# Performance work log

Hardware: AMD Instinct MI355X
Metric: run time of the kernel (lower is better)

## Reference

```python
import jax, jax.numpy as jnp
import numpy as np

B, T, H, V = 32, 16, 768, 32000
EPS = 1e-5


def _conv(x, w, stride, pad):
    return jax.lax.conv_general_dilated(
        x, w, (stride, stride), [(pad, pad), (pad, pad)],
        dimension_numbers=('NCHW', 'OIHW', 'NCHW'))


def _bn(x, g, b, m, v):
    inv = g / jnp.sqrt(v + EPS)
    return x * inv[None, :, None, None] + (b - m * inv)[None, :, None, None]


def setup_inputs() -> dict:
    key = jax.random.key(0)
    ks = iter(jax.random.split(key, 48))

    def rn(shape, s=0.02):
        return s * jax.random.normal(next(ks), shape, jnp.float32)

    def bn_params(c):
        g = 1.0 + 0.1 * jax.random.normal(next(ks), (c,), jnp.float32)
        b = 0.1 * jax.random.normal(next(ks), (c,), jnp.float32)
        m = 0.1 * jax.random.normal(next(ks), (c,), jnp.float32)
        v = jax.random.uniform(next(ks), (c,), jnp.float32, 0.5, 1.5)
        return g, b, m, v

    inp = {}
    inp['images'] = jax.random.normal(next(ks), (B, 3, 224, 224), jnp.float32)
    inp['captions'] = jax.random.randint(next(ks), (B, T), 0, V)

    inp['conv1_w'] = rn((64, 3, 7, 7))
    inp['bn1_g'], inp['bn1_b'], inp['bn1_m'], inp['bn1_v'] = bn_params(64)
    inp['conv2_w'] = rn((128, 64, 3, 3))
    inp['bn2_g'], inp['bn2_b'], inp['bn2_m'], inp['bn2_v'] = bn_params(128)
    inp['conv3_w'] = rn((256, 128, 3, 3))
    inp['bn3_g'], inp['bn3_b'], inp['bn3_m'], inp['bn3_v'] = bn_params(256)
    inp['conv4_w'] = rn((H, 256, 3, 3))
    inp['bn4_g'], inp['bn4_b'], inp['bn4_m'], inp['bn4_v'] = bn_params(H)

    emb = rn((V, H), 1.0)
    inp['emb_table'] = emb.at[0].set(0.0)  # padding_idx=0 row is zero
    inp['attn_w'] = rn((H, H))             # attn_proj (no bias)
    inp['w_ih'] = rn((4 * H, 2 * H))       # LSTM input weights (i,f,g,o)
    inp['w_hh'] = rn((4 * H, H))
    inp['b_ih'] = rn((4 * H,))
    inp['b_hh'] = rn((4 * H,))
    inp['fc_w'] = rn((V, H))
    inp['fc_b'] = rn((V,))
    return inp


def _forward(images, captions, conv1_w, bn1_g, bn1_b, bn1_m, bn1_v,
             conv2_w, bn2_g, bn2_b, bn2_m, bn2_v,
             conv3_w, bn3_g, bn3_b, bn3_m, bn3_v,
             conv4_w, bn4_g, bn4_b, bn4_m, bn4_v,
             emb_table, attn_w, w_ih, w_hh, b_ih, b_hh, fc_w, fc_b):
    # ---- ResNetEncoder ----
    x = jax.nn.relu(_bn(_conv(images, conv1_w, 2, 3), bn1_g, bn1_b, bn1_m, bn1_v))
    x = jax.lax.reduce_window(x, -jnp.inf, jax.lax.max, (1, 1, 3, 3), (1, 1, 2, 2),
                              ((0, 0), (0, 0), (1, 1), (1, 1)))
    x = jax.nn.relu(_bn(_conv(x, conv2_w, 1, 1), bn2_g, bn2_b, bn2_m, bn2_v))
    x = jax.nn.relu(_bn(_conv(x, conv3_w, 2, 1), bn3_g, bn3_b, bn3_m, bn3_v))
    x = jax.nn.relu(_bn(_conv(x, conv4_w, 1, 1), bn4_g, bn4_b, bn4_m, bn4_v))
    b, c, hh, ww = x.shape
    memory = x.reshape(b, c, hh * ww).transpose(0, 2, 1)[:, :196, :]  # [B,196,H]

    # ---- LSTMAttnDecoder ----
    emb = emb_table[captions]  # [B,T,H]
    h0 = jnp.zeros((b, H), jnp.float32)
    c0 = jnp.zeros((b, H), jnp.float32)

    def step(carry, e_t):
        h, cst = carry
        q = h @ attn_w.T                                    # [B,H]
        scores = jnp.einsum('bh,bmh->bm', q, memory)        # [B,196]
        ctx = jnp.einsum('bm,bmh->bh', jax.nn.softmax(scores, axis=-1), memory)
        xin = jnp.concatenate([e_t, ctx], axis=-1)          # [B,2H]
        gates = xin @ w_ih.T + b_ih + h @ w_hh.T + b_hh     # [B,4H]
        i, f, g, o = jnp.split(gates, 4, axis=-1)
        c_new = jax.nn.sigmoid(f) * cst + jax.nn.sigmoid(i) * jnp.tanh(g)
        h_new = jax.nn.sigmoid(o) * jnp.tanh(c_new)
        logits = h_new @ fc_w.T + fc_b                      # [B,V]
        return (h_new, c_new), logits

    (hT, cT), logits = jax.lax.scan(step, (h0, c0), emb.transpose(1, 0, 2))
    logits = logits.transpose(1, 0, 2)  # [B,T,V]
    return logits, (hT[None], cT[None])


def reference(images, captions, conv1_w, bn1_g, bn1_b, bn1_m, bn1_v,
              conv2_w, bn2_g, bn2_b, bn2_m, bn2_v,
              conv3_w, bn3_g, bn3_b, bn3_m, bn3_v,
              conv4_w, bn4_g, bn4_b, bn4_m, bn4_v,
              emb_table, attn_w, w_ih, w_hh, b_ih, b_hh, fc_w, fc_b):
    return _forward(images, captions, conv1_w, bn1_g, bn1_b, bn1_m, bn1_v,
                    conv2_w, bn2_g, bn2_b, bn2_m, bn2_v,
                    conv3_w, bn3_g, bn3_b, bn3_m, bn3_v,
                    conv4_w, bn4_g, bn4_b, bn4_m, bn4_v,
                    emb_table, attn_w, w_ih, w_hh, b_ih, b_hh, fc_w, fc_b)
```

## Files before the change

### kernel.cpp

```cpp
#include <hip/hip_runtime.h>
#include <math.h>

#define NB 32
#define NT 16
#define NH 768
#define NV 32000

typedef short bf16x8 __attribute__((ext_vector_type(8)));
typedef float floatx4 __attribute__((ext_vector_type(4)));
typedef unsigned short ushort_t;

__device__ __forceinline__ float bf2f(unsigned short h) {
    unsigned u = ((unsigned)h) << 16;
    return __builtin_bit_cast(float, u);
}
__device__ __forceinline__ unsigned short f2bf(float f) {
    unsigned u = __builtin_bit_cast(unsigned, f);
    u += 0x7fffu + ((u >> 16) & 1u);
    return (unsigned short)(u >> 16);
}
__device__ __forceinline__ float sigmoidf_(float x) { return 1.f / (1.f + expf(-x)); }

__device__ __forceinline__ int swz8(int bid, int N) {
    return (bid & 7) * (N >> 3) + (bid >> 3);
}

__device__ __forceinline__ bf16x8 cvt8(float4 a, float4 b) {
    bf16x8 t;
    t[0] = (short)f2bf(a.x); t[1] = (short)f2bf(a.y);
    t[2] = (short)f2bf(a.z); t[3] = (short)f2bf(a.w);
    t[4] = (short)f2bf(b.x); t[5] = (short)f2bf(b.y);
    t[6] = (short)f2bf(b.z); t[7] = (short)f2bf(b.w);
    return t;
}

__global__ __launch_bounds__(256) void bn_prep4(
    const float* __restrict__ g1, const float* __restrict__ b1, const float* __restrict__ m1, const float* __restrict__ v1,
    const float* __restrict__ g2, const float* __restrict__ b2, const float* __restrict__ m2, const float* __restrict__ v2,
    const float* __restrict__ g3, const float* __restrict__ b3, const float* __restrict__ m3, const float* __restrict__ v3,
    const float* __restrict__ g4, const float* __restrict__ b4, const float* __restrict__ m4, const float* __restrict__ v4,
    float* __restrict__ s1, float* __restrict__ o1, float* __restrict__ s2, float* __restrict__ o2,
    float* __restrict__ s3, float* __restrict__ o3, float* __restrict__ s4, float* __restrict__ o4) {
    int i = blockIdx.x * 256 + threadIdx.x;
    const float *g, *b, *m, *v;
    float *s, *o;
    int c;
    if (i < 64)        { g = g1; b = b1; m = m1; v = v1; s = s1; o = o1; c = i; }
    else if (i < 192)  { g = g2; b = b2; m = m2; v = v2; s = s2; o = o2; c = i - 64; }
    else if (i < 448)  { g = g3; b = b3; m = m3; v = v3; s = s3; o = o3; c = i - 192; }
    else if (i < 1216) { g = g4; b = b4; m = m4; v = v4; s = s4; o = o4; c = i - 448; }
    else return;
    float inv = g[c] * rsqrtf(v[c] + 1e-5f);
    s[c] = inv;
    o[c] = b[c] - m[c] * inv;
}

__global__ __launch_bounds__(256) void zfill(unsigned long long* __restrict__ p, long long n) {
    long long i = (long long)blockIdx.x * 256 + threadIdx.x;
    if (i < n) p[i] = 0ULL;
}

__global__ __launch_bounds__(256) void cvt_b16rows(const float* __restrict__ src, ushort_t* __restrict__ dst,
                                                   int cols8, int ldsrc, int total8) {
    int i = blockIdx.x * 256 + threadIdx.x;
    if (i >= total8) return;
    int r = i / cols8, g = i % cols8;
    const float4* s = (const float4*)(src + (size_t)r * ldsrc + g * 8);
    float4 a = s[0], b = s[1];
    *(bf16x8*)(dst + (size_t)i * 8) = cvt8(a, b);
}

__global__ __launch_bounds__(256) void cvt_packW_conv(const float* __restrict__ w, ushort_t* __restrict__ dst,
                                                      int CIN, int total) {
    int idx = blockIdx.x * 256 + threadIdx.x;
    if (idx >= total) return;
    int e = idx & 7, lane = (idx >> 3) & 63, j = (idx >> 9) & 3;
    int r = idx >> 11;
    int KQ = CIN >> 5;
    int kq = r % KQ; r /= KQ;
    int tap = r % 9; int nt = r / 9;
    int co = nt * 64 + j * 16 + (lane & 15);
    int ci = kq * 32 + (lane >> 4) * 8 + e;
    dst[idx] = f2bf(w[((size_t)co * CIN + ci) * 9 + tap]);
}

__global__ __launch_bounds__(256) void cvt_wcombP(const float* __restrict__ w_ih, const float* __restrict__ w_hh,
                                                  ushort_t* __restrict__ dst) {
    int idx = blockIdx.x * 256 + threadIdx.x;
    if (idx >= 3072 * 1536) return;
    int e = idx & 7, lane = (idx >> 3) & 63;
    int t = idx >> 9;
    int kq = t % 48, gg = t / 48;
    int g = gg & 3, bx = gg >> 2;
    int j = g * 768 + bx * 16 + (lane & 15);
    int k = kq * 32 + (lane >> 4) * 8 + e;
    float v = (k < NH) ? w_ih[(size_t)j * (2 * NH) + NH + k] : w_hh[(size_t)j * NH + (k - NH)];
    dst[idx] = f2bf(v);
}

__global__ __launch_bounds__(256) void cvt_wattnTP(const float* __restrict__ w, ushort_t* __restrict__ dst) {
    int idx = blockIdx.x * 256 + threadIdx.x;
    if (idx >= 768 * 768) return;
    int e = idx & 7, lane = (idx >> 3) & 63, j = (idx >> 9) & 3;
    int t = idx >> 11;
    int kq = t % 24, nt = t / 24;
    int n = nt * 64 + 16 * j + (lane & 15);
    int k = kq * 32 + (lane >> 4) * 8 + e;
    dst[idx] = f2bf(w[(size_t)k * 768 + n]);
}

__global__ __launch_bounds__(256) void cvt_pad(const float* __restrict__ src, ushort_t* __restrict__ dst) {
    int idx = blockIdx.x * 256 + threadIdx.x;
    if (idx >= 64 * 160) return;
    int co = idx / 160, k = idx % 160;
    dst[idx] = (k < 147) ? f2bf(src[co * 147 + k]) : (ushort_t)0;
}

__global__ __launch_bounds__(256) void im2col1(const float* __restrict__ img, ushort_t* __restrict__ A) {
    int idx = blockIdx.x * 256 + threadIdx.x;
    const int total = 121856 * 160;
    if (idx >= total) return;
    int k = idx % 160;
    int m = idx / 160;
    ushort_t v = 0;
    if (k < 147) {
        int b = m / 3808;
        int rm = m % 3808;
        int y = rm / 112, x = rm % 112;
        int ci = k / 49;
        int r = k % 49;
        int ky = r / 7, kx = r % 7;
        int iy = 2 * y - 3 + ky;
        int ix = 2 * x - 3 + kx;
        if ((unsigned)iy < 224u && (unsigned)ix < 224u)
            v = f2bf(img[((size_t)(b * 3 + ci) * 224 + iy) * 224 + ix]);
    }
    A[idx] = v;
}

__global__ __launch_bounds__(256) void conv1_gemm(
    const ushort_t* __restrict__ A, const ushort_t* __restrict__ Bw,
    const float* __restrict__ scale, const float* __restrict__ bias,
    ushort_t* __restrict__ out) {
    int lane = threadIdx.x & 63, w = threadIdx.x >> 6;
    int m0 = (blockIdx.x * 4 + w) * 64;
    int lr = lane & 15, kl = (lane >> 4) * 8;
    floatx4 acc[4][4];
    #pragma unroll
    for (int i = 0; i < 4; ++i)
        #pragma unroll
        for (int j = 0; j < 4; ++j) acc[i][j] = 0.f;
    #pragma unroll
    for (int k0 = 0; k0 < 160; k0 += 32) {
        bf16x8 a[4], bb[4];
        #pragma unroll
        for (int i = 0; i < 4; ++i) a[i] = *(const bf16x8*)(A + (size_t)(m0 + 16 * i + lr) * 160 + kl + k0);
        #pragma unroll
        for (int j = 0; j < 4; ++j) bb[j] = *(const bf16x8*)(Bw + (size_t)(16 * j + lr) * 160 + kl + k0);
        #pragma unroll
        for (int i = 0; i < 4; ++i)
            #pragma unroll
            for (int j = 0; j < 4; ++j)
                acc[i][j] = __builtin_amdgcn_mfma_f32_16x16x32_bf16(a[i], bb[j], acc[i][j], 0, 0, 0);
    }
    #pragma unroll
    for (int i = 0; i < 4; ++i) {
        #pragma unroll
        for (int r = 0; r < 4; ++r) {
            int m = m0 + 16 * i + (lane >> 4) * 4 + r;
            int b = m / 3808;
            int rm = m % 3808;
            int y = rm / 112, x = rm % 112;
            #pragma unroll
            for (int j = 0; j < 4; ++j) {
                int n = 16 * j + lr;
                float v = fmaxf(acc[i][j][r] * scale[n] + bias[n], 0.f);
                out[((size_t)(b * 34 + y) * 112 + x) * 64 + n] = f2bf(v);
            }
        }
    }
}

__global__ __launch_bounds__(256) void pool_kernel(const ushort_t* __restrict__ in,
                                                   ushort_t* __restrict__ hal2) {
    int idx = blockIdx.x * 256 + threadIdx.x;
    const int total = 32 * 17 * 56 * 8;
    if (idx >= total) return;
    int c8 = idx & 7;
    int rest = idx >> 3;
    int x = rest % 56; rest /= 56;
    int y = rest % 17; int b = rest / 17;
    float mx[8];
    #pragma unroll
    for (int j = 0; j < 8; ++j) mx[j] = -INFINITY;
    for (int dy = -1; dy <= 1; ++dy) {
        int iy = 2 * y + dy;
        if ((unsigned)iy >= 34u) continue;
        for (int dx = -1; dx <= 1; ++dx) {
            int ix = 2 * x + dx;
            if ((unsigned)ix >= 112u) continue;
            bf16x8 v = *(const bf16x8*)(in + (((size_t)(b * 34 + iy)) * 112 + ix) * 64 + c8 * 8);
            #pragma unroll
            for (int j = 0; j < 8; ++j) mx[j] = fmaxf(mx[j], bf2f((unsigned short)v[j]));
        }
    }
    bf16x8 o;
    #pragma unroll
    for (int j = 0; j < 8; ++j) o[j] = (short)f2bf(mx[j]);
    *(bf16x8*)(hal2 + (((size_t)(b * 19 + y + 1)) * 58 + (x + 1)) * 64 + c8 * 8) = o;
}

template <int CIN, int HH, int WH, int STRIDE, int HOUT, int WOUT, int COUT, int MEMOUT, int OH, int OW>
__global__ __launch_bounds__(64) void conv_mfma(
    const ushort_t* __restrict__ in, const ushort_t* __restrict__ wtP,
    const float* __restrict__ scale, const float* __restrict__ bias,
    ushort_t* __restrict__ out) {
    const int KQ = CIN / 32;
    const int NK = 9 * KQ;
    const int MT = (32 * HOUT * WOUT) / 64;
    const int NTL = COUT / 64;
    int id = swz8(blockIdx.x, MT * NTL);
    int mt = id % MT, nt = id / MT;
    int lane = threadIdx.x;
    int lr = lane & 15, kl = (lane >> 4) * 8;
    int rowoff[4];
    #pragma unroll
    for (int i = 0; i < 4; ++i) {
        int m = mt * 64 + 16 * i + lr;
        int b = m / (HOUT * WOUT);
        int rm = m % (HOUT * WOUT);
        int y = rm / WOUT, x = rm % WOUT;
        rowoff[i] = ((b * HH + y * STRIDE) * WH + x * STRIDE) * CIN + kl;
    }
    floatx4 acc[4][4];
    #pragma unroll
    for (int i = 0; i < 4; ++i)
        #pragma unroll
        for (int j = 0; j < 4; ++j) acc[i][j] = 0.f;

    auto ioffOf = [&](int ks) {
        int tap = ks / KQ;
        int k0 = (ks & (KQ - 1)) * 32;
        int ky = tap / 3, kx = tap - ky * 3;
        return (ky * WH + kx) * CIN + k0;
    };
    const ushort_t* bbase = wtP + ((size_t)nt * 9 * KQ * 4 * 64 + lane) * 8;

    bf16x8 aC[4], bC[4], aN[4], bN[4];
    {
        int io = ioffOf(0);
        #pragma unroll
        for (int i = 0; i < 4; ++i) aC[i] = *(const bf16x8*)(in + rowoff[i] + io);
        #pragma unroll
        for (int j = 0; j < 4; ++j) bC[j] = *(const bf16x8*)(bbase + ((size_t)(0 * 4 + j) * 64) * 8);
    }
    for (int ks = 0; ks < NK; ks += 2) {
        {
            int io = ioffOf(ks + 1);
            #pragma unroll
            for (int i = 0; i < 4; ++i) aN[i] = *(const bf16x8*)(in + rowoff[i] + io);
            #pragma unroll
            for (int j = 0; j < 4; ++j) bN[j] = *(const bf16x8*)(bbase + ((size_t)((ks + 1) * 4 + j) * 64) * 8);
        }
        #pragma unroll
        for (int i = 0; i < 4; ++i)
            #pragma unroll
            for (int j = 0; j < 4; ++j)
                acc[i][j] = __builtin_amdgcn_mfma_f32_16x16x32_bf16(aC[i], bC[j], acc[i][j], 0, 0, 0);
        if (ks + 2 < NK) {
            int io = ioffOf(ks + 2);
            #pragma unroll
            for (int i = 0; i < 4; ++i) aC[i] = *(const bf16x8*)(in + rowoff[i] + io);
            #pragma unroll
            for (int j = 0; j < 4; ++j) bC[j] = *(const bf16x8*)(bbase + ((size_t)((ks + 2) * 4 + j) * 64) * 8);
        }
        #pragma unroll
        for (int i = 0; i < 4; ++i)
            #pragma unroll
            for (int j = 0; j < 4; ++j)
                acc[i][j] = __builtin_amdgcn_mfma_f32_16x16x32_bf16(aN[i], bN[j], acc[i][j], 0, 0, 0);
    }
    #pragma unroll
    for (int i = 0; i < 4; ++i) {
        #pragma unroll
        for (int r = 0; r < 4; ++r) {
            int m = mt * 64 + 16 * i + (lane >> 4) * 4 + r;
            int b = m / (HOUT * WOUT);
            int rm = m % (HOUT * WOUT);
            int y = rm / WOUT, x = rm % WOUT;
            #pragma unroll
            for (int j = 0; j < 4; ++j) {
                int n = nt * 64 + 16 * j + lr;
                float v = fmaxf(acc[i][j][r] * scale[n] + bias[n], 0.f);
                ushort_t hv = f2bf(v);
                if (MEMOUT) {
                    out[(size_t)m * COUT + n] = hv;
                } else {
                    out[((size_t)(b * OH + y + 1) * OW + (x + 1)) * COUT + n] = hv;
                }
            }
        }
    }
}

__global__ __launch_bounds__(64) void kmat_gemm(
    const ushort_t* __restrict__ memv, const ushort_t* __restrict__ Bp,
    ushort_t* __restrict__ KT) {
    int id = swz8(blockIdx.x, 98 * 12);
    int mt = id % 98, nt = id / 98;
    int lane = threadIdx.x;
    int lr = lane & 15, kl = (lane >> 4) * 8;
    const ushort_t* arow[4];
    #pragma unroll
    for (int i = 0; i < 4; ++i) arow[i] = memv + (size_t)(mt * 64 + 16 * i + lr) * 768 + kl;
    const ushort_t* bbase = Bp + ((size_t)nt * 24 * 4 * 64 + lane) * 8;
    floatx4 acc[4][4];
    #pragma unroll
    for (int i = 0; i < 4; ++i)
        #pragma unroll
        for (int j = 0; j < 4; ++j) acc[i][j] = 0.f;
    bf16x8 aC[4], bC[4], aN[4], bN[4];
    #pragma unroll
    for (int i = 0; i < 4; ++i) aC[i] = *(const bf16x8*)(arow[i]);
    #pragma unroll
    for (int j = 0; j < 4; ++j) bC[j] = *(const bf16x8*)(bbase + ((size_t)j * 64) * 8);
    for (int ks = 0; ks < 24; ks += 2) {
        #pragma unroll
        for (int i = 0; i < 4; ++i) aN[i] = *(const bf16x8*)(arow[i] + (ks + 1) * 32);
        #pragma unroll
        for (int j = 0; j < 4; ++j) bN[j] = *(const bf16x8*)(bbase + ((size_t)((ks + 1) * 4 + j) * 64) * 8);
        #pragma unroll
        for (int i = 0; i < 4; ++i)
            #pragma unroll
            for (int j = 0; j < 4; ++j)
                acc[i][j] = __builtin_amdgcn_mfma_f32_16x16x32_bf16(aC[i], bC[j], acc[i][j], 0, 0, 0);
        if (ks + 2 < 24) {
            #pragma unroll
            for (int i = 0; i < 4; ++i) aC[i] = *(const bf16x8*)(arow[i] + (ks + 2) * 32);
            #pragma unroll
            for (int j = 0; j < 4; ++j) bC[j] = *(const bf16x8*)(bbase + ((size_t)((ks + 2) * 4 + j) * 64) * 8);
        }
        #pragma unroll
        for (int i = 0; i < 4; ++i)
            #pragma unroll
            for (int j = 0; j < 4; ++j)
                acc[i][j] = __builtin_amdgcn_mfma_f32_16x16x32_bf16(aN[i], bN[j], acc[i][j], 0, 0, 0);
    }
    #pragma unroll
    for (int i = 0; i < 4; ++i) {
        #pragma unroll
        for (int r = 0; r < 4; ++r) {
            int mg = mt * 64 + 16 * i + (lane >> 4) * 4 + r;
            int b = mg / 196, m = mg % 196;
            #pragma unroll
            for (int j = 0; j < 4; ++j) {
                int n = nt * 64 + 16 * j + lr;
                KT[(((size_t)b * 96 + (n >> 3)) * 196 + m) * 8 + (n & 7)] = f2bf(acc[i][j][r]);
            }
        }
    }
}

__global__ __launch_bounds__(256) void gather_embP(const int* __restrict__ caps,
                                                   const float* __restrict__ table,
                                                   ushort_t* __restrict__ dst) {
    int idx = blockIdx.x * 256 + threadIdx.x;
    if (idx >= 512 * 768) return;
    int e = idx & 7, lane = (idx >> 3) & 63, i = (idx >> 9) & 3;
    int t2 = idx >> 11;
    int kq = t2 % 24, mt = t2 / 24;
    int r = mt * 64 + i * 16 + (lane & 15);
    int k = kq * 32 + (lane >> 4) * 8 + e;
    int t = r >> 5, b = r & 31;
    dst[idx] = f2bf(table[(size_t)caps[b * NT + t] * NH + k]);
}

template <int REMAP>
__global__ __launch_bounds__(256, 4) void gemm_ldsb(
    const ushort_t* __restrict__ Ap, const ushort_t* __restrict__ Bb,
    const float* __restrict__ bias1, const float* __restrict__ bias2,
    float* __restrict__ C, int N) {
    __shared__ ushort_t bt[2][64 * 72];
    int tid = threadIdx.x;
    int lane = tid & 63, w = tid >> 6;
    int nblk = (N >> 6) * 2;
    int id = swz8(blockIdx.x, nblk);
    int nt = id >> 1, mh = id & 1;
    int n0 = nt * 64;
    int mt = mh * 4 + w;
    int lr = lane & 15, hi = lane >> 4;
    int srow = tid >> 2, sc = tid & 3;
    const ushort_t* gsrc = Bb + (size_t)(n0 + srow) * 768 + sc * 8;
    int woff = srow * 72 + sc * 8;
    floatx4 acc[4][4];
    #pragma unroll
    for (int i = 0; i < 4; ++i)
        #pragma unroll
        for (int j = 0; j < 4; ++j) acc[i][j] = 0.f;
    bf16x8 s0 = *(const bf16x8*)(gsrc);
    bf16x8 s1 = *(const bf16x8*)(gsrc + 32);
    for (int kc = 0; kc < 12; ++kc) {
        ushort_t* bufw = &bt[kc & 1][0];
        *(bf16x8*)(bufw + woff) = s0;
        *(bf16x8*)(bufw + woff + 32) = s1;
        if (kc < 11) {
            const ushort_t* p = gsrc + (size_t)(kc + 1) * 64;
            s0 = *(const bf16x8*)(p);
            s1 = *(const bf16x8*)(p + 32);
        }
        __syncthreads();
        const ushort_t* bufr = &bt[kc & 1][0];
        #pragma unroll
        for (int kk = 0; kk < 2; ++kk) {
            int kq = kc * 2 + kk;
            bf16x8 bfr[4], a[4];
            #pragma unroll
            for (int j = 0; j < 4; ++j)
                bfr[j] = *(const bf16x8*)(bufr + (j * 16 + lr) * 72 + kk * 32 + hi * 8);
            #pragma unroll
            for (int i = 0; i < 4; ++i)
                a[i] = *(const bf16x8*)(Ap + ((((size_t)mt * 24 + kq) * 4 + i) * 64 + lane) * 8);
            #pragma unroll
            for (int i = 0; i < 4; ++i)
                #pragma unroll
                for (int j = 0; j < 4; ++j)
                    acc[i][j] = __builtin_amdgcn_mfma_f32_16x16x32_bf16(a[i], bfr[j], acc[i][j], 0, 0, 0);
        }
    }
    #pragma unroll
    for (int i = 0; i < 4; ++i) {
        #pragma unroll
        for (int rr = 0; rr < 4; ++rr) {
            int m = mt * 64 + 16 * i + hi * 4 + rr;
            #pragma unroll
            for (int j = 0; j < 4; ++j) {
                int n = n0 + 16 * j + lr;
                float vv = acc[i][j][rr];
                if (bias1) vv += bias1[n];
                if (bias2) vv += bias2[n];
                if (REMAP) {
                    int t = m >> 5, b = m & 31;
                    C[(size_t)((b << 4) + t) * NV + n] = vv;
                } else {
                    C[(size_t)m * N + n] = vv;
                }
            }
        }
    }
}

__global__ __launch_bounds__(768) void attn2(
    ushort_t* __restrict__ xin, const ushort_t* __restrict__ KT,
    const ushort_t* __restrict__ mem) {
    __shared__ float hq[NH];
    __shared__ float sl[196];
    __shared__ float red[16];
    int b = blockIdx.x, tid = threadIdx.x;
    hq[tid] = bf2f(xin[(size_t)b * 1536 + NH + tid]);
    __syncthreads();
    if (tid < 392) {
        int m = tid >> 1, half = tid & 1;
        const ushort_t* basep = KT + (((size_t)b * 96 + half * 48) * 196 + m) * 8;
        float acc = 0.f;
        #pragma unroll 4
        for (int k8 = 0; k8 < 48; ++k8) {
            bf16x8 v = *(const bf16x8*)(basep + (size_t)k8 * 196 * 8);
            const float* qp = hq + (half * 48 + k8) * 8;
            #pragma unroll
            for (int j = 0; j < 8; ++j)
                acc = fmaf(bf2f((unsigned short)v[j]), qp[j], acc);
        }
        acc += __shfl_xor(acc, 1);
        if (!half) sl[m] = acc;
    }
    __syncthreads();
    float sc = (tid < 196) ? sl[tid] : -INFINITY;
    float v = sc;
    #pragma unroll
    for (int off = 32; off; off >>= 1) v = fmaxf(v, __shfl_down(v, off));
    if ((tid & 63) == 0) red[tid >> 6] = v;
    __syncthreads();
    if (tid == 0) {
        float m = red[0];
        for (int i = 1; i < 12; ++i) m = fmaxf(m, red[i]);
        red[12] = m;
    }
    __syncthreads();
    float mx = red[12];
    float e = (tid < 196) ? expf(sc - mx) : 0.f;
    __syncthreads();
    v = e;
    #pragma unroll
    for (int off = 32; off; off >>= 1) v += __shfl_down(v, off);
    if ((tid & 63) == 0) red[tid >> 6] = v;
    __syncthreads();
    if (tid == 0) {
        float s = red[0];
        for (int i = 1; i < 12; ++i) s += red[i];
        red[12] = 1.f / s;
    }
    __syncthreads();
    if (tid < 196) sl[tid] = e * red[12];
    __syncthreads();
    {
        float acc = 0.f;
        const ushort_t* mb = mem + (size_t)b * 196 * NH + tid;
        #pragma unroll 4
        for (int m = 0; m < 196; ++m) acc = fmaf(sl[m], bf2f(mb[(size_t)m * NH]), acc);
        xin[(size_t)b * 1536 + tid] = f2bf(acc);
    }
}

__global__ __launch_bounds__(256) void step_fused(
    const ushort_t* __restrict__ xin_r, const ushort_t* __restrict__ wcombP,
    const float* __restrict__ eg_t,
    float* __restrict__ cbuf, float* __restrict__ hbuf,
    ushort_t* __restrict__ xin_w, ushort_t* __restrict__ hallP, int tstep) {
    __shared__ float pbuf[4][64][33];
    int lane = threadIdx.x & 63, w = threadIdx.x >> 6;
    int bx = blockIdx.x;
    int lr = lane & 15, kl = (lane >> 4) * 8;
    floatx4 acc[2][4];
    #pragma unroll
    for (int i = 0; i < 2; ++i)
        #pragma unroll
        for (int g = 0; g < 4; ++g) acc[i][g] = 0.f;
    for (int kq = 0; kq < 12; ++kq) {
        int k = w * 384 + kq * 32;
        bf16x8 a[2], bb[4];
        #pragma unroll
        for (int i = 0; i < 2; ++i)
            a[i] = *(const bf16x8*)(xin_r + (size_t)(16 * i + lr) * 1536 + k + kl);
        #pragma unroll
        for (int g = 0; g < 4; ++g)
            bb[g] = *(const bf16x8*)(wcombP + (((size_t)(bx * 4 + g) * 48 + (w * 12 + kq)) * 64 + lane) * 8);
        #pragma unroll
        for (int i = 0; i < 2; ++i)
            #pragma unroll
            for (int g = 0; g < 4; ++g)
                acc[i][g] = __builtin_amdgcn_mfma_f32_16x16x32_bf16(a[i], bb[g], acc[i][g], 0, 0, 0);
    }
    #pragma unroll
    for (int i = 0; i < 2; ++i)
        #pragma unroll
        for (int g = 0; g < 4; ++g)
            #pragma unroll
            for (int r = 0; r < 4; ++r) {
                int m = 16 * i + (lane >> 4) * 4 + r;
                pbuf[w][g * 16 + lr][m] = acc[i][g][r];
            }
    __syncthreads();
    int tid = threadIdx.x;
    #pragma unroll
    for (int o = 0; o < 2; ++o) {
        int pid = tid * 2 + o;
        int m = pid & 31, c = pid >> 5;
        int kcol = bx * 16 + c;
        float gi = 0.f, gf = 0.f, gg = 0.f, go = 0.f;
        #pragma unroll
        for (int ww = 0; ww < 4; ++ww) {
            gi += pbuf[ww][c][m];
            gf += pbuf[ww][16 + c][m];
            gg += pbuf[ww][32 + c][m];
            go += pbuf[ww][48 + c][m];
        }
        const float* eg = eg_t + (size_t)m * 3072;
        gi += eg[kcol];
        gf += eg[768 + kcol];
        gg += eg[1536 + kcol];
        go += eg[2304 + kcol];
        float cst = cbuf[m * 768 + kcol];
        float cn = sigmoidf_(gf) * cst + sigmoidf_(gi) * tanhf(gg);
        float hn = sigmoidf_(go) * tanhf(cn);
        cbuf[m * 768 + kcol] = cn;
        hbuf[m * 768 + kcol] = hn;
        ushort_t hb = f2bf(hn);
        xin_w[(size_t)m * 1536 + NH + kcol] = hb;
        int rrow = tstep * 32 + m;
        int mtp = rrow >> 6, ip = (rrow >> 4) & 3, lrp = rrow & 15;
        int kqp = kcol >> 5, hip = (kcol >> 3) & 3, ep = kcol & 7;
        hallP[((((size_t)mtp * 24 + kqp) * 4 + ip) * 64 + (lrp | (hip << 4))) * 8 + ep] = hb;
    }
}

__global__ __launch_bounds__(256) void zero_state(float* __restrict__ h, float* __restrict__ c,
                                                  ushort_t* __restrict__ xin) {
    int i = blockIdx.x * 256 + threadIdx.x;
    if (i < NB * 1536) xin[i] = 0;
    if (i < NB * NH) { h[i] = 0.f; c[i] = 0.f; }
}

__global__ __launch_bounds__(256) void copy_hc(const float* __restrict__ h, const float* __restrict__ c,
                                               float* __restrict__ out) {
    int i = blockIdx.x * 256 + threadIdx.x;
    if (i < NB * NH) {
        out[(size_t)NB * NT * NV + i] = h[i];
        out[(size_t)NB * NT * NV + NB * NH + i] = c[i];
    }
}

extern "C" void kernel_launch(void* const* d_in, const int* in_sizes, int n_in,
                              void* d_out, int out_size, void* d_ws, size_t ws_size,
                              hipStream_t stream) {
    const float* images   = (const float*)d_in[0];
    const int*   captions = (const int*)d_in[1];
    const float* conv1_w  = (const float*)d_in[2];
    const float* bn1_g = (const float*)d_in[3], *bn1_b = (const float*)d_in[4];
    const float* bn1_m = (const float*)d_in[5], *bn1_v = (const float*)d_in[6];
    const float* conv2_w  = (const float*)d_in[7];
    const float* bn2_g = (const float*)d_in[8], *bn2_b = (const float*)d_in[9];
    const float* bn2_m = (const float*)d_in[10], *bn2_v = (const float*)d_in[11];
    const float* conv3_w  = (const float*)d_in[12];
    const float* bn3_g = (const float*)d_in[13], *bn3_b = (const float*)d_in[14];
    const float* bn3_m = (const float*)d_in[15], *bn3_v = (const float*)d_in[16];
    const float* conv4_w  = (const float*)d_in[17];
    const float* bn4_g = (const float*)d_in[18], *bn4_b = (const float*)d_in[19];
    const float* bn4_m = (const float*)d_in[20], *bn4_v = (const float*)d_in[21];
    const float* emb_table = (const float*)d_in[22];
    const float* attn_w   = (const float*)d_in[23];
    const float* w_ih     = (const float*)d_in[24];
    const float* w_hh     = (const float*)d_in[25];
    const float* b_ih     = (const float*)d_in[26];
    const float* b_hh     = (const float*)d_in[27];
    const float* fc_w     = (const float*)d_in[28];
    const float* fc_b     = (const float*)d_in[29];
    float* out = (float*)d_out;

    char* base = (char*)d_ws;
    size_t off = 0;
    auto alloc = [&](size_t bytes) { char* p = base + off; off += (bytes + 255) & ~(size_t)255; return p; };
    float* s1 = (float*)alloc(64 * 4);   float* bb1 = (float*)alloc(64 * 4);
    float* s2 = (float*)alloc(128 * 4);  float* bb2 = (float*)alloc(128 * 4);
    float* s3 = (float*)alloc(256 * 4);  float* bb3 = (float*)alloc(256 * 4);
    float* s4 = (float*)alloc(768 * 4);  float* bb4 = (float*)alloc(768 * 4);
    ushort_t* c1out = (ushort_t*)alloc((size_t)32 * 34 * 112 * 64 * 2);
    size_t halo_start = off;
    ushort_t* hal2 = (ushort_t*)alloc((size_t)32 * 19 * 58 * 64 * 2);
    ushort_t* hal3 = (ushort_t*)alloc((size_t)32 * 18 * 58 * 128 * 2);
    ushort_t* hal4 = (ushort_t*)alloc((size_t)32 * 10 * 30 * 256 * 2);
    size_t halo_bytes = off - halo_start;
    ushort_t* memv = (ushort_t*)alloc((size_t)32 * 196 * 768 * 2);
    ushort_t* KT   = (ushort_t*)alloc((size_t)32 * 96 * 196 * 8 * 2);
    ushort_t* wb1 = (ushort_t*)alloc((size_t)64 * 160 * 2);
    ushort_t* wb2 = (ushort_t*)alloc((size_t)128 * 9 * 64 * 2);
    ushort_t* wb3 = (ushort_t*)alloc((size_t)256 * 9 * 128 * 2);
    ushort_t* wb4 = (ushort_t*)alloc((size_t)768 * 9 * 256 * 2);
    ushort_t* wattnTP = (ushort_t*)alloc((size_t)768 * 768 * 2);
    ushort_t* wcombP = (ushort_t*)alloc((size_t)3072 * 1536 * 2);
    ushort_t* wihL = (ushort_t*)alloc((size_t)3072 * 768 * 2);
    ushort_t* e512P = (ushort_t*)alloc((size_t)512 * 768 * 2);
    float* eg   = (float*)alloc((size_t)512 * 3072 * 4);
    ushort_t* HallP = (ushort_t*)alloc((size_t)512 * 768 * 2);
    float* hbuf = (float*)alloc(NB * NH * 4);
    float* cbuf = (float*)alloc(NB * NH * 4);
    ushort_t* xinA = (ushort_t*)alloc((size_t)NB * 1536 * 2);
    ushort_t* xinB = (ushort_t*)alloc((size_t)NB * 1536 * 2);
    char* ubig = alloc((size_t)NV * NH * 2);
    ushort_t* imcol = (ushort_t*)ubig;
    ushort_t* fcwb  = (ushort_t*)ubig;

    bn_prep4<<<5, 256, 0, stream>>>(bn1_g, bn1_b, bn1_m, bn1_v,
                                    bn2_g, bn2_b, bn2_m, bn2_v,
                                    bn3_g, bn3_b, bn3_m, bn3_v,
                                    bn4_g, bn4_b, bn4_m, bn4_v,
                                    s1, bb1, s2, bb2, s3, bb3, s4, bb4);
    cvt_pad<<<(64 * 160 + 255) / 256, 256, 0, stream>>>(conv1_w, wb1);
    cvt_packW_conv<<<(128 * 9 * 64 + 255) / 256, 256, 0, stream>>>(conv2_w, wb2, 64, 128 * 9 * 64);
    cvt_packW_conv<<<(256 * 9 * 128 + 255) / 256, 256, 0, stream>>>(conv3_w, wb3, 128, 256 * 9 * 128);
    cvt_packW_conv<<<(768 * 9 * 256 + 255) / 256, 256, 0, stream>>>(conv4_w, wb4, 256, 768 * 9 * 256);
    cvt_wattnTP<<<(768 * 768 + 255) / 256, 256, 0, stream>>>(attn_w, wattnTP);
    cvt_wcombP<<<(3072 * 1536 + 255) / 256, 256, 0, stream>>>(w_ih, w_hh, wcombP);
    cvt_b16rows<<<(3072 * 96 + 255) / 256, 256, 0, stream>>>(w_ih, wihL, 96, 1536, 3072 * 96);
    {
        long long n8 = (long long)(halo_bytes / 8);
        zfill<<<(unsigned)((n8 + 255) / 256), 256, 0, stream>>>((unsigned long long*)hal2, n8);
    }

    im2col1<<<(121856 * 160 + 255) / 256, 256, 0, stream>>>(images, imcol);
    conv1_gemm<<<476, 256, 0, stream>>>(imcol, wb1, s1, bb1, c1out);
    cvt_b16rows<<<(NV * 96 + 255) / 256, 256, 0, stream>>>(fc_w, fcwb, 96, 768, NV * 96);
    pool_kernel<<<(32 * 17 * 56 * 8 + 255) / 256, 256, 0, stream>>>(c1out, hal2);
    conv_mfma<64, 19, 58, 1, 16, 56, 128, 0, 18, 58>
        <<<896, 64, 0, stream>>>(hal2, wb2, s2, bb2, hal3);
    conv_mfma<128, 18, 58, 2, 8, 28, 256, 0, 10, 30>
        <<<448, 64, 0, stream>>>(hal3, wb3, s3, bb3, hal4);
    conv_mfma<256, 10, 30, 1, 7, 28, 768, 1, 1, 1>
        <<<1176, 64, 0, stream>>>(hal4, wb4, s4, bb4, memv);

    kmat_gemm<<<1176, 64, 0, stream>>>(memv, wattnTP, KT);

    gather_embP<<<(512 * 768) / 256, 256, 0, stream>>>(captions, emb_table, e512P);
    gemm_ldsb<0><<<96, 256, 0, stream>>>(e512P, wihL, b_ih, b_hh, eg, 3072);
    zero_state<<<(NB * 1536 + 255) / 256, 256, 0, stream>>>(hbuf, cbuf, xinA);

    ushort_t* xcur = xinA;
    ushort_t* xnxt = xinB;
    for (int t = 0; t < NT; ++t) {
        attn2<<<NB, NH, 0, stream>>>(xcur, KT, memv);
        step_fused<<<48, 256, 0, stream>>>(
            xcur, wcombP, eg + (size_t)t * NB * 3072, cbuf, hbuf, xnxt, HallP, t);
        ushort_t* tmp = xcur; xcur = xnxt; xnxt = tmp;
    }

    gemm_ldsb<1><<<1000, 256, 0, stream>>>(HallP, fcwb, fc_b, nullptr, out, NV);

    copy_hc<<<(NB * NH + 255) / 256, 256, 0, stream>>>(hbuf, cbuf, out);
}
```

Measured before the change: 904.6 us.

## Merge prep kernels into one launch and split conv4 over taps with reduction

```diff
diff --git a/kernel.cpp b/kernel.cpp
--- a/kernel.cpp
+++ b/kernel.cpp
@@ -34,86 +34,105 @@
     return t;
 }
 
-__global__ __launch_bounds__(256) void bn_prep4(
+#define SEG0 1216
+#define SEG1 (SEG0 + 10240)
+#define SEG2 (SEG1 + 73728)
+#define SEG3 (SEG2 + 294912)
+#define SEG4 (SEG3 + 1769472)
+#define SEG5 (SEG4 + 589824)
+#define SEG6 (SEG5 + 4718592)
+#define SEG7 (SEG6 + 294912)
+#define SEG8 (SEG7 + 393216)
+#define SEG9 (SEG8 + 49152)
+__global__ __launch_bounds__(256) void prep_all(
     const float* __restrict__ g1, const float* __restrict__ b1, const float* __restrict__ m1, const float* __restrict__ v1,
     const float* __restrict__ g2, const float* __restrict__ b2, const float* __restrict__ m2, const float* __restrict__ v2,
     const float* __restrict__ g3, const float* __restrict__ b3, const float* __restrict__ m3, const float* __restrict__ v3,
     const float* __restrict__ g4, const float* __restrict__ b4, const float* __restrict__ m4, const float* __restrict__ v4,
     float* __restrict__ s1, float* __restrict__ o1, float* __restrict__ s2, float* __restrict__ o2,
-    float* __restrict__ s3, float* __restrict__ o3, float* __restrict__ s4, float* __restrict__ o4) {
-    int i = blockIdx.x * 256 + threadIdx.x;
-    const float *g, *b, *m, *v;
-    float *s, *o;
-    int c;
-    if (i < 64)        { g = g1; b = b1; m = m1; v = v1; s = s1; o = o1; c = i; }
-    else if (i < 192)  { g = g2; b = b2; m = m2; v = v2; s = s2; o = o2; c = i - 64; }
-    else if (i < 448)  { g = g3; b = b3; m = m3; v = v3; s = s3; o = o3; c = i - 192; }
-    else if (i < 1216) { g = g4; b = b4; m = m4; v = v4; s = s4; o = o4; c = i - 448; }
-    else return;
-    float inv = g[c] * rsqrtf(v[c] + 1e-5f);
-    s[c] = inv;
-    o[c] = b[c] - m[c] * inv;
-}
-
-__global__ __launch_bounds__(256) void zfill(unsigned long long* __restrict__ p, long long n) {
-    long long i = (long long)blockIdx.x * 256 + threadIdx.x;
-    if (i < n) p[i] = 0ULL;
-}
-
-__global__ __launch_bounds__(256) void cvt_b16rows(const float* __restrict__ src, ushort_t* __restrict__ dst,
-                                                   int cols8, int ldsrc, int total8) {
-    int i = blockIdx.x * 256 + threadIdx.x;
-    if (i >= total8) return;
-    int r = i / cols8, g = i % cols8;
-    const float4* s = (const float4*)(src + (size_t)r * ldsrc + g * 8);
-    float4 a = s[0], b = s[1];
-    *(bf16x8*)(dst + (size_t)i * 8) = cvt8(a, b);
-}
-
-__global__ __launch_bounds__(256) void cvt_packW_conv(const float* __restrict__ w, ushort_t* __restrict__ dst,
-                                                      int CIN, int total) {
-    int idx = blockIdx.x * 256 + threadIdx.x;
-    if (idx >= total) return;
-    int e = idx & 7, lane = (idx >> 3) & 63, j = (idx >> 9) & 3;
-    int r = idx >> 11;
-    int KQ = CIN >> 5;
-    int kq = r % KQ; r /= KQ;
-    int tap = r % 9; int nt = r / 9;
-    int co = nt * 64 + j * 16 + (lane & 15);
-    int ci = kq * 32 + (lane >> 4) * 8 + e;
-    dst[idx] = f2bf(w[((size_t)co * CIN + ci) * 9 + tap]);
-}
-
-__global__ __launch_bounds__(256) void cvt_wcombP(const float* __restrict__ w_ih, const float* __restrict__ w_hh,
-                                                  ushort_t* __restrict__ dst) {
-    int idx = blockIdx.x * 256 + threadIdx.x;
-    if (idx >= 3072 * 1536) return;
-    int e = idx & 7, lane = (idx >> 3) & 63;
-    int t = idx >> 9;
-    int kq = t % 48, gg = t / 48;
-    int g = gg & 3, bx = gg >> 2;
-    int j = g * 768 + bx * 16 + (lane & 15);
-    int k = kq * 32 + (lane >> 4) * 8 + e;
-    float v = (k < NH) ? w_ih[(size_t)j * (2 * NH) + NH + k] : w_hh[(size_t)j * NH + (k - NH)];
-    dst[idx] = f2bf(v);
-}
-
-__global__ __launch_bounds__(256) void cvt_wattnTP(const float* __restrict__ w, ushort_t* __restrict__ dst) {
-    int idx = blockIdx.x * 256 + threadIdx.x;
-    if (idx >= 768 * 768) return;
-    int e = idx & 7, lane = (idx >> 3) & 63, j = (idx >> 9) & 3;
-    int t = idx >> 11;
-    int kq = t % 24, nt = t / 24;
-    int n = nt * 64 + 16 * j + (lane & 15);
-    int k = kq * 32 + (lane >> 4) * 8 + e;
-    dst[idx] = f2bf(w[(size_t)k * 768 + n]);
-}
-
-__global__ __launch_bounds__(256) void cvt_pad(const float* __restrict__ src, ushort_t* __restrict__ dst) {
-    int idx = blockIdx.x * 256 + threadIdx.x;
-    if (idx >= 64 * 160) return;
-    int co = idx / 160, k = idx % 160;
-    dst[idx] = (k < 147) ? f2bf(src[co * 147 + k]) : (ushort_t)0;
+    float* __restrict__ s3, float* __restrict__ o3, float* __restrict__ s4, float* __restrict__ o4,
+    const float* __restrict__ conv1_w, ushort_t* __restrict__ wb1,
+    const float* __restrict__ conv2_w, ushort_t* __restrict__ wb2,
+    const float* __restrict__ conv3_w, ushort_t* __restrict__ wb3,
+    const float* __restrict__ conv4_w, ushort_t* __restrict__ wb4,
+    const float* __restrict__ attn_w, ushort_t* __restrict__ wattnTP,
+    const float* __restrict__ w_ih, const float* __restrict__ w_hh, ushort_t* __restrict__ wcombP,
+    ushort_t* __restrict__ wihL,
+    const int* __restrict__ caps, const float* __restrict__ table, ushort_t* __restrict__ e512P,
+    float* __restrict__ hbuf, float* __restrict__ cbuf, ushort_t* __restrict__ xinA,
+    unsigned long long* __restrict__ halo, long long n8) {
+    long long gi = (long long)blockIdx.x * 256 + threadIdx.x;
+    if (gi < SEG0) {
+        int i = (int)gi;
+        const float *g, *b, *m, *v;
+        float *s, *o;
+        int c;
+        if (i < 64)        { g = g1; b = b1; m = m1; v = v1; s = s1; o = o1; c = i; }
+        else if (i < 192)  { g = g2; b = b2; m = m2; v = v2; s = s2; o = o2; c = i - 64; }
+        else if (i < 448)  { g = g3; b = b3; m = m3; v = v3; s = s3; o = o3; c = i - 192; }
+        else               { g = g4; b = b4; m = m4; v = v4; s = s4; o = o4; c = i - 448; }
+        float inv = g[c] * rsqrtf(v[c] + 1e-5f);
+        s[c] = inv;
+        o[c] = b[c] - m[c] * inv;
+    } else if (gi < SEG1) {
+        int idx = (int)(gi - SEG0);
+        int co = idx / 160, k = idx % 160;
+        wb1[idx] = (k < 147) ? f2bf(conv1_w[co * 147 + k]) : (ushort_t)0;
+    } else if (gi < SEG4) {
+        const float* w;
+        ushort_t* dst;
+        int CIN, idx;
+        if (gi < SEG2)      { w = conv2_w; dst = wb2; CIN = 64;  idx = (int)(gi - SEG1); }
+        else if (gi < SEG3) { w = conv3_w; dst = wb3; CIN = 128; idx = (int)(gi - SEG2); }
+        else                { w = conv4_w; dst = wb4; CIN = 256; idx = (int)(gi - SEG3); }
+        int e = idx & 7, lane = (idx >> 3) & 63, j = (idx >> 9) & 3;
+        int r = idx >> 11;
+        int KQ = CIN >> 5;
+        int kq = r % KQ; r /= KQ;
+        int tap = r % 9; int nt = r / 9;
+        int co = nt * 64 + j * 16 + (lane & 15);
+        int ci = kq * 32 + (lane >> 4) * 8 + e;
+        dst[idx] = f2bf(w[((size_t)co * CIN + ci) * 9 + tap]);
+    } else if (gi < SEG5) {
+        int idx = (int)(gi - SEG4);
+        int e = idx & 7, lane = (idx >> 3) & 63, j = (idx >> 9) & 3;
+        int t = idx >> 11;
+        int kq = t % 24, nt = t / 24;
+        int n = nt * 64 + 16 * j + (lane & 15);
+        int k = kq * 32 + (lane >> 4) * 8 + e;
+        wattnTP[idx] = f2bf(attn_w[(size_t)k * 768 + n]);
+    } else if (gi < SEG6) {
+        int idx = (int)(gi - SEG5);
+        int e = idx & 7, lane = (idx >> 3) & 63;
+        int t = idx >> 9;
+        int kq = t % 48, gg = t / 48;
+        int g = gg & 3, bx = gg >> 2;
+        int j = g * 768 + bx * 16 + (lane & 15);
+        int k = kq * 32 + (lane >> 4) * 8 + e;
+        float v = (k < NH) ? w_ih[(size_t)j * (2 * NH) + NH + k] : w_hh[(size_t)j * NH + (k - NH)];
+        wcombP[idx] = f2bf(v);
+    } else if (gi < SEG7) {
+        int idx = (int)(gi - SEG6);
+        int r = idx / 96, g = idx % 96;
+        const float4* s = (const float4*)(w_ih + (size_t)r * 1536 + g * 8);
+        *(bf16x8*)(wihL + (size_t)idx * 8) = cvt8(s[0], s[1]);
+    } else if (gi < SEG8) {
+        int idx = (int)(gi - SEG7);
+        int e = idx & 7, lane = (idx >> 3) & 63, i = (idx >> 9) & 3;
+        int t2 = idx >> 11;
+        int kq = t2 % 24, mt = t2 / 24;
+        int r = mt * 64 + i * 16 + (lane & 15);
+        int k = kq * 32 + (lane >> 4) * 8 + e;
+        int t = r >> 5, b = r & 31;
+        e512P[idx] = f2bf(table[(size_t)caps[b * NT + t] * NH + k]);
+    } else if (gi < SEG9) {
+        int i = (int)(gi - SEG8);
+        xinA[i] = 0;
+        if (i < NB * NH) { hbuf[i] = 0.f; cbuf[i] = 0.f; }
+    } else {
+        long long j = gi - SEG9;
+        if (j < n8) halo[j] = 0ULL;
+    }
 }
 
 __global__ __launch_bounds__(256) void im2col1(const float* __restrict__ img, ushort_t* __restrict__ A) {
@@ -138,6 +157,15 @@
     A[idx] = v;
 }
 
+__global__ __launch_bounds__(256) void cvt_b16rows(const float* __restrict__ src, ushort_t* __restrict__ dst,
+                                                   int cols8, int ldsrc, int total8) {
+    int i = blockIdx.x * 256 + threadIdx.x;
+    if (i >= total8) return;
+    int r = i / cols8, g = i % cols8;
+    const float4* s = (const float4*)(src + (size_t)r * ldsrc + g * 8);
+    *(bf16x8*)(dst + (size_t)i * 8) = cvt8(s[0], s[1]);
+}
+
 __global__ __launch_bounds__(256) void conv1_gemm(
     const ushort_t* __restrict__ A, const ushort_t* __restrict__ Bw,
     const float* __restrict__ scale, const float* __restrict__ bias,
@@ -210,7 +238,7 @@
     *(bf16x8*)(hal2 + (((size_t)(b * 19 + y + 1)) * 58 + (x + 1)) * 64 + c8 * 8) = o;
 }
 
-template <int CIN, int HH, int WH, int STRIDE, int HOUT, int WOUT, int COUT, int MEMOUT, int OH, int OW>
+template <int CIN, int HH, int WH, int STRIDE, int HOUT, int WOUT, int COUT, int OH, int OW>
 __global__ __launch_bounds__(64) void conv_mfma(
     const ushort_t* __restrict__ in, const ushort_t* __restrict__ wtP,
     const float* __restrict__ scale, const float* __restrict__ bias,
@@ -252,7 +280,7 @@
         #pragma unroll
         for (int i = 0; i < 4; ++i) aC[i] = *(const bf16x8*)(in + rowoff[i] + io);
         #pragma unroll
-        for (int j = 0; j < 4; ++j) bC[j] = *(const bf16x8*)(bbase + ((size_t)(0 * 4 + j) * 64) * 8);
+        for (int j = 0; j < 4; ++j) bC[j] = *(const bf16x8*)(bbase + ((size_t)j * 64) * 8);
     }
     for (int ks = 0; ks < NK; ks += 2) {
         {
@@ -292,15 +320,114 @@
             for (int j = 0; j < 4; ++j) {
                 int n = nt * 64 + 16 * j + lr;
                 float v = fmaxf(acc[i][j][r] * scale[n] + bias[n], 0.f);
-                ushort_t hv = f2bf(v);
-                if (MEMOUT) {
-                    out[(size_t)m * COUT + n] = hv;
-                } else {
-                    out[((size_t)(b * OH + y + 1) * OW + (x + 1)) * COUT + n] = hv;
-                }
+                out[((size_t)(b * OH + y + 1) * OW + (x + 1)) * COUT + n] = f2bf(v);
             }
         }
     }
+}
+
+__global__ __launch_bounds__(64) void conv4_split(
+    const ushort_t* __restrict__ in, const ushort_t* __restrict__ wtP,
+    float* __restrict__ part) {
+    const int CIN = 256, HH = 10, WH = 30, HOUT = 7, WOUT = 28;
+    int id = swz8(blockIdx.x, 98 * 12 * 3);
+    int s = id / (98 * 12);
+    int rem = id % (98 * 12);
+    int nt = rem / 98, mt = rem % 98;
+    int lane = threadIdx.x;
+    int lr = lane & 15, kl = (lane >> 4) * 8;
+    int rowoff[4];
+    #pragma unroll
+    for (int i = 0; i < 4; ++i) {
+        int m = mt * 64 + 16 * i + lr;
+        int b = m / (HOUT * WOUT);
+        int rm = m % (HOUT * WOUT);
+        int y = rm / WOUT, x = rm % WOUT;
+        rowoff[i] = ((b * HH + y) * WH + x) * CIN + kl;
+    }
+    floatx4 acc[4][4];
+    #pragma unroll
+    for (int i = 0; i < 4; ++i)
+        #pragma unroll
+        for (int j = 0; j < 4; ++j) acc[i][j] = 0.f;
+
+    auto ioffOf = [&](int ks) {
+        int tap = s * 3 + (ks >> 3);
+        int k0 = (ks & 7) * 32;
+        int ky = tap / 3, kx = tap - ky * 3;
+        return (ky * WH + kx) * CIN + k0;
+    };
+    const ushort_t* bbase = wtP + ((size_t)nt * 9 * 8 * 4 * 64 + lane) * 8;
+    auto bOf = [&](int ks, int j) {
+        return (const bf16x8*)(bbase + ((size_t)((s * 24 + ks) * 4 + j) * 64) * 8);
+    };
+
+    bf16x8 aC[4], bC[4], aN[4], bN[4];
+    {
+        int io = ioffOf(0);
+        #pragma unroll
+        for (int i = 0; i < 4; ++i) aC[i] = *(const bf16x8*)(in + rowoff[i] + io);
+        #pragma unroll
+        for (int j = 0; j < 4; ++j) bC[j] = *bOf(0, j);
+    }
+    for (int ks = 0; ks < 24; ks += 2) {
+        {
+            int io = ioffOf(ks + 1);
+            #pragma unroll
+            for (int i = 0; i < 4; ++i) aN[i] = *(const bf16x8*)(in + rowoff[i] + io);
+            #pragma unroll
+            for (int j = 0; j < 4; ++j) bN[j] = *bOf(ks + 1, j);
+        }
+        #pragma unroll
+        for (int i = 0; i < 4; ++i)
+            #pragma unroll
+            for (int j = 0; j < 4; ++j)
+                acc[i][j] = __builtin_amdgcn_mfma_f32_16x16x32_bf16(aC[i], bC[j], acc[i][j], 0, 0, 0);
+        if (ks + 2 < 24) {
+            int io = ioffOf(ks + 2);
+            #pragma unroll
+            for (int i = 0; i < 4; ++i) aC[i] = *(const bf16x8*)(in + rowoff[i] + io);
+            #pragma unroll
+            for (int j = 0; j < 4; ++j) bC[j] = *bOf(ks + 2, j);
+        }
+        #pragma unroll
+        for (int i = 0; i < 4; ++i)
+            #pragma unroll
+            for (int j = 0; j < 4; ++j)
+                acc[i][j] = __builtin_amdgcn_mfma_f32_16x16x32_bf16(aN[i], bN[j], acc[i][j], 0, 0, 0);
+    }
+    float* pbase = part + (size_t)s * 6272 * 768;
+    #pragma unroll
+    for (int i = 0; i < 4; ++i) {
+        #pragma unroll
+        for (int r = 0; r < 4; ++r) {
+            int m = mt * 64 + 16 * i + (lane >> 4) * 4 + r;
+            #pragma unroll
+            for (int j = 0; j < 4; ++j) {
+                int n = nt * 64 + 16 * j + lr;
+                pbase[(size_t)m * 768 + n] = acc[i][j][r];
+            }
+        }
+    }
+}
+
+__global__ __launch_bounds__(256) void comb4(
+    const float* __restrict__ part, const float* __restrict__ scale, const float* __restrict__ bias,
+    ushort_t* __restrict__ memv) {
+    int idx = blockIdx.x * 256 + threadIdx.x;
+    if (idx >= 6272 * 192) return;
+    int m = idx / 192, nq = idx % 192;
+    int n = nq * 4;
+    size_t off = (size_t)m * 768 + n;
+    const float4 a = *(const float4*)(part + off);
+    const float4 b = *(const float4*)(part + (size_t)6272 * 768 + off);
+    const float4 c = *(const float4*)(part + (size_t)2 * 6272 * 768 + off);
+    ushort_t o[4];
+    o[0] = f2bf(fmaxf((a.x + b.x + c.x) * scale[n]     + bias[n],     0.f));
+    o[1] = f2bf(fmaxf((a.y + b.y + c.y) * scale[n + 1] + bias[n + 1], 0.f));
+    o[2] = f2bf(fmaxf((a.z + b.z + c.z) * scale[n + 2] + bias[n + 2], 0.f));
+    o[3] = f2bf(fmaxf((a.w + b.w + c.w) * scale[n + 3] + bias[n + 3], 0.f));
+    *(unsigned long long*)(memv + off) = *(unsigned long long*)o;
 }
 
 __global__ __launch_bounds__(64) void kmat_gemm(
@@ -359,20 +486,6 @@
             }
         }
     }
-}
-
-__global__ __launch_bounds__(256) void gather_embP(const int* __restrict__ caps,
-                                                   const float* __restrict__ table,
-                                                   ushort_t* __restrict__ dst) {
-    int idx = blockIdx.x * 256 + threadIdx.x;
-    if (idx >= 512 * 768) return;
-    int e = idx & 7, lane = (idx >> 3) & 63, i = (idx >> 9) & 3;
-    int t2 = idx >> 11;
-    int kq = t2 % 24, mt = t2 / 24;
-    int r = mt * 64 + i * 16 + (lane & 15);
-    int k = kq * 32 + (lane >> 4) * 8 + e;
-    int t = r >> 5, b = r & 31;
-    dst[idx] = f2bf(table[(size_t)caps[b * NT + t] * NH + k]);
 }
 
 template <int REMAP>
@@ -581,13 +694,6 @@
         int kqp = kcol >> 5, hip = (kcol >> 3) & 3, ep = kcol & 7;
         hallP[((((size_t)mtp * 24 + kqp) * 4 + ip) * 64 + (lrp | (hip << 4))) * 8 + ep] = hb;
     }
-}
-
-__global__ __launch_bounds__(256) void zero_state(float* __restrict__ h, float* __restrict__ c,
-                                                  ushort_t* __restrict__ xin) {
-    int i = blockIdx.x * 256 + threadIdx.x;
-    if (i < NB * 1536) xin[i] = 0;
-    if (i < NB * NH) { h[i] = 0.f; c[i] = 0.f; }
 }
 
 __global__ __launch_bounds__(256) void copy_hc(const float* __restrict__ h, const float* __restrict__ c,
@@ -655,43 +761,37 @@
     float* cbuf = (float*)alloc(NB * NH * 4);
     ushort_t* xinA = (ushort_t*)alloc((size_t)NB * 1536 * 2);
     ushort_t* xinB = (ushort_t*)alloc((size_t)NB * 1536 * 2);
+    float* part = (float*)alloc((size_t)3 * 6272 * 768 * 4);
     char* ubig = alloc((size_t)NV * NH * 2);
     ushort_t* imcol = (ushort_t*)ubig;
     ushort_t* fcwb  = (ushort_t*)ubig;
 
-    bn_prep4<<<5, 256, 0, stream>>>(bn1_g, bn1_b, bn1_m, bn1_v,
-                                    bn2_g, bn2_b, bn2_m, bn2_v,
-                                    bn3_g, bn3_b, bn3_m, bn3_v,
-                                    bn4_g, bn4_b, bn4_m, bn4_v,
-                                    s1, bb1, s2, bb2, s3, bb3, s4, bb4);
-    cvt_pad<<<(64 * 160 + 255) / 256, 256, 0, stream>>>(conv1_w, wb1);
-    cvt_packW_conv<<<(128 * 9 * 64 + 255) / 256, 256, 0, stream>>>(conv2_w, wb2, 64, 128 * 9 * 64);
-    cvt_packW_conv<<<(256 * 9 * 128 + 255) / 256, 256, 0, stream>>>(conv3_w, wb3, 128, 256 * 9 * 128);
-    cvt_packW_conv<<<(768 * 9 * 256 + 255) / 256, 256, 0, stream>>>(conv4_w, wb4, 256, 768 * 9 * 256);
-    cvt_wattnTP<<<(768 * 768 + 255) / 256, 256, 0, stream>>>(attn_w, wattnTP);
-    cvt_wcombP<<<(3072 * 1536 + 255) / 256, 256, 0, stream>>>(w_ih, w_hh, wcombP);
-    cvt_b16rows<<<(3072 * 96 + 255) / 256, 256, 0, stream>>>(w_ih, wihL, 96, 1536, 3072 * 96);
-    {
-        long long n8 = (long long)(halo_bytes / 8);
-        zfill<<<(unsigned)((n8 + 255) / 256), 256, 0, stream>>>((unsigned long long*)hal2, n8);
-    }
+    long long n8 = (long long)(halo_bytes / 8);
+    long long prep_total = (long long)SEG9 + n8;
+    prep_all<<<(unsigned)((prep_total + 255) / 256), 256, 0, stream>>>(
+        bn1_g, bn1_b, bn1_m, bn1_v, bn2_g, bn2_b, bn2_m, bn2_v,
+        bn3_g, bn3_b, bn3_m, bn3_v, bn4_g, bn4_b, bn4_m, bn4_v,
+        s1, bb1, s2, bb2, s3, bb3, s4, bb4,
+        conv1_w, wb1, conv2_w, wb2, conv3_w, wb3, conv4_w, wb4,
+        attn_w, wattnTP, w_ih, w_hh, wcombP, wihL,
+        captions, emb_table, e512P,
+        hbuf, cbuf, xinA,
+        (unsigned long long*)hal2, n8);
+
+    gemm_ldsb<0><<<96, 256, 0, stream>>>(e512P, wihL, b_ih, b_hh, eg, 3072);
 
     im2col1<<<(121856 * 160 + 255) / 256, 256, 0, stream>>>(images, imcol);
     conv1_gemm<<<476, 256, 0, stream>>>(imcol, wb1, s1, bb1, c1out);
     cvt_b16rows<<<(NV * 96 + 255) / 256, 256, 0, stream>>>(fc_w, fcwb, 96, 768, NV * 96);
     pool_kernel<<<(32 * 17 * 56 * 8 + 255) / 256, 256, 0, stream>>>(c1out, hal2);
-    conv_mfma<64, 19, 58, 1, 16, 56, 128, 0, 18, 58>
+    conv_mfma<64, 19, 58, 1, 16, 56, 128, 18, 58>
         <<<896, 64, 0, stream>>>(hal2, wb2, s2, bb2, hal3);
-    conv_mfma<128, 18, 58, 2, 8, 28, 256, 0, 10, 30>
+    conv_mfma<128, 18, 58, 2, 8, 28, 256, 10, 30>
         <<<448, 64, 0, stream>>>(hal3, wb3, s3, bb3, hal4);
-    conv_mfma<256, 10, 30, 1, 7, 28, 768, 1, 1, 1>
-        <<<1176, 64, 0, stream>>>(hal4, wb4, s4, bb4, memv);
+    conv4_split<<<3528, 64, 0, stream>>>(hal4, wb4, part);
+    comb4<<<(6272 * 192 + 255) / 256, 256, 0, stream>>>(part, s4, bb4, memv);
 
     kmat_gemm<<<1176, 64, 0, stream>>>(memv, wattnTP, KT);
-
-    gather_embP<<<(512 * 768) / 256, 256, 0, stream>>>(captions, emb_table, e512P);
-    gemm_ldsb<0><<<96, 256, 0, stream>>>(e512P, wihL, b_ih, b_hh, eg, 3072);
-    zero_state<<<(NB * 1536 + 255) / 256, 256, 0, stream>>>(hbuf, cbuf, xinA);
 
     ushort_t* xcur = xinA;
     ushort_t* xnxt = xinB;
```

New measurement: 902.4 us. Within noise of the previous version (-0.2%).
